# Performance work log

Measured on AMD Instinct MI355X. Metric: run time of the kernel, lower is better.

The kernel has to match this reference:

```python
import jax, jax.numpy as jnp
import numpy as np

N, D_IN = 16384, 1024
E, K = 16, 2
D_EMB, H_UNITS, D_HID = 128, 1024, 512


def setup_inputs() -> dict:
    key = jax.random.key(0)
    ks = jax.random.split(key, 10)
    s = lambda fan_in: 1.0 / np.sqrt(fan_in)
    return {
        "x": jax.random.normal(ks[0], (N, D_IN), jnp.float32),
        "Wr": jax.random.normal(ks[1], (D_IN, D_EMB), jnp.float32) * s(D_IN),
        "br": jnp.zeros((D_EMB,), jnp.float32),
        "expert_embeddings": jax.random.normal(ks[2], (E, D_EMB), jnp.float32) * s(D_EMB),
        "W1": jax.random.normal(ks[3], (E, D_IN, H_UNITS), jnp.float32) * s(D_IN),
        "b1": jnp.zeros((E, H_UNITS), jnp.float32),
        "W2": jax.random.normal(ks[4], (E, H_UNITS, H_UNITS // 2), jnp.float32) * s(H_UNITS),
        "b2": jnp.zeros((E, H_UNITS // 2), jnp.float32),
        "W3": jax.random.normal(ks[5], (E, H_UNITS // 2, D_HID), jnp.float32) * s(H_UNITS // 2),
        "b3": jnp.zeros((E, D_HID), jnp.float32),
    }


def reference(x, Wr, br, expert_embeddings, W1, b1, W2, b2, W3, b3):
    # Router: query per token [N, D_EMB]
    q = x @ Wr + br
    # Negative squared L2 distance to each expert embedding -> scores [N, E]
    d2 = jnp.sum(jnp.square(q[:, None, :] - expert_embeddings[None, :, :]), axis=-1)
    scores = -d2
    # Top-k gating (softmax over the k selected scores only)
    top_k_scores, top_k_idx = jax.lax.top_k(scores, K)        # [N, K]
    gates = jax.nn.softmax(top_k_scores, axis=-1)             # [N, K]
    # Dense all-expert MLP (as the original: every expert on every token)
    h1 = jax.nn.relu(jnp.einsum('nd,edh->enh', x, W1) + b1[:, None, :])   # [E,N,1024]
    h2 = jax.nn.relu(jnp.einsum('enh,ehm->enm', h1, W2) + b2[:, None, :]) # [E,N,512]
    eo = jnp.einsum('enm,emo->eno', h2, W3) + b3[:, None, :]              # [E,N,D_HID]
    eo_t = jnp.transpose(eo, (1, 0, 2))                                   # [N,E,D_HID]
    # Gather top-k expert outputs per token and combine with gates
    sel = jnp.take_along_axis(eo_t, top_k_idx[:, :, None], axis=1)        # [N,K,D_HID]
    combined = jnp.sum(sel * gates[:, :, None], axis=1)                   # [N,D_HID]
    return combined
```

## Files before the change

### kernel.cpp

```cpp
#include <hip/hip_runtime.h>

typedef unsigned short u16;
typedef __attribute__((ext_vector_type(8))) short short8;
typedef __attribute__((ext_vector_type(4))) float f32x4;

#define N_TOK 16384
#define DIN   1024
#define NE    16
#define DEMB  128
#define H1N   1024
#define H2N   512
#define DOUT  512
#define CAP   34816
#define MT    (CAP/128)
#define RBLK  1024

#define OFF_P      0ul
#define OFF_C      65536ul
#define OFF_CTRL   65792ul
#define OFF_E01    66048ul
#define OFF_G01    197120ul
#define OFF_GTOK   328192ul
#define OFF_GGATE  467456ul
#define OFF_TSLOT  606720ul
#define OFF_BH     737792ul
#define OFF_BB     803328ul
#define OFF_W1T    868864ul
#define OFF_W2T    34423296ul
#define OFF_W3T    51200512ul
#define OFF_XBF    59589120ul
#define OFF_H1     93143552ul
#define OFF_H2     164446720ul
#define OFF_EO     OFF_H1

__device__ __forceinline__ u16 f2bf(float f) {
  union { float f; unsigned u; } v; v.f = f;
  unsigned r = v.u + 0x7fff + ((v.u >> 16) & 1);
  return (u16)(r >> 16);
}

__device__ __forceinline__ void async_copy16(const u16* g, u16* l) {
  __builtin_amdgcn_global_load_lds((const __attribute__((address_space(1))) unsigned*)g,
                                   (__attribute__((address_space(3))) unsigned*)l,
                                   16, 0, 0);
}

__global__ void router_prep(const float* __restrict__ Wr, const float* __restrict__ br,
                            const float* __restrict__ emb, float* __restrict__ P,
                            float* __restrict__ c) {
  int idx = blockIdx.x * 256 + threadIdx.x;
  int row = idx >> 4, e = idx & 15;
  float s = 0.f;
  for (int j = 0; j < DEMB; ++j) s += Wr[row * DEMB + j] * emb[e * DEMB + j];
  P[row * NE + e] = 2.f * s;
  if (idx < NE) {
    float cc = 0.f, n2 = 0.f;
    for (int j = 0; j < DEMB; ++j) {
      float ev = emb[idx * DEMB + j];
      cc += br[j] * ev;
      n2 += ev * ev;
    }
    c[idx] = 2.f * cc - n2;
  }
}

__global__ void __launch_bounds__(256) router_score(
    const float* __restrict__ x, const float* __restrict__ P,
    const float* __restrict__ c, int* __restrict__ e01,
    float* __restrict__ g01, int* __restrict__ bhist,
    u16* __restrict__ xbf) {
  __shared__ float xs[16384];
  __shared__ int lh[16];
  int wave = threadIdx.x >> 6, lane = threadIdx.x & 63;
  int e2 = lane & 7, kgl = lane >> 3;
  int tbase = blockIdx.x * 16 + wave * 4;
  float* xw = xs + wave * 4096;

  if (threadIdx.x < 16) lh[threadIdx.x] = 0;

  u16* xbrow = xbf + (size_t)tbase * DIN;
  #pragma unroll
  for (int t = 0; t < 4; ++t) {
    const float* src = x + (size_t)(tbase + t) * DIN;
    #pragma unroll
    for (int q = 0; q < 4; ++q) {
      int g = q * 256 + lane * 4;
      float4 v = *(const float4*)(src + g);
      *(float4*)(xw + t * 1024 + g) = v;
      ushort4 o;
      o.x = f2bf(v.x); o.y = f2bf(v.y); o.z = f2bf(v.z); o.w = f2bf(v.w);
      *(ushort4*)(xbrow + t * DIN + g) = o;
    }
  }
  __syncthreads();

  int te0 = 2 * e2, te1 = te0 + 1;
  float ce0 = c[te0], ce1 = c[te1];
  const float* Pb = P + te0;

  float acc0[4] = {0.f, 0.f, 0.f, 0.f};
  float acc1[4] = {0.f, 0.f, 0.f, 0.f};
  int cbase = kgl * 128;
  #pragma unroll 4
  for (int i = 0; i < 32; ++i) {
    int w = (kgl * 4 + i * 4) & 127;
    int idx = cbase + w;
    float2 pv0 = *(const float2*)(Pb + (size_t)(idx + 0) * NE);
    float2 pv1 = *(const float2*)(Pb + (size_t)(idx + 1) * NE);
    float2 pv2 = *(const float2*)(Pb + (size_t)(idx + 2) * NE);
    float2 pv3 = *(const float2*)(Pb + (size_t)(idx + 3) * NE);
    #pragma unroll
    for (int t = 0; t < 4; ++t) {
      float4 xv = *(const float4*)(xw + t * 1024 + idx);
      acc0[t] = fmaf(xv.x, pv0.x, acc0[t]); acc1[t] = fmaf(xv.x, pv0.y, acc1[t]);
      acc0[t] = fmaf(xv.y, pv1.x, acc0[t]); acc1[t] = fmaf(xv.y, pv1.y, acc1[t]);
      acc0[t] = fmaf(xv.z, pv2.x, acc0[t]); acc1[t] = fmaf(xv.z, pv2.y, acc1[t]);
      acc0[t] = fmaf(xv.w, pv3.x, acc0[t]); acc1[t] = fmaf(xv.w, pv3.y, acc1[t]);
    }
  }

  for (int t = 0; t < 4; ++t) {
    float s0 = acc0[t], s1 = acc1[t];
    #pragma unroll
    for (int off = 8; off <= 32; off <<= 1) {
      s0 += __shfl_xor(s0, off);
      s1 += __shfl_xor(s1, off);
    }
    s0 += ce0; s1 += ce1;
    float hi; int hidx;
    if (s0 >= s1) { hi = s0; hidx = te0; } else { hi = s1; hidx = te1; }
    float m1 = hi; int i1 = hidx;
    #pragma unroll
    for (int off = 1; off < 8; off <<= 1) {
      float so = __shfl_xor(m1, off); int io = __shfl_xor(i1, off);
      if (so > m1 || (so == m1 && io < i1)) { m1 = so; i1 = io; }
    }
    float c2; int c2i;
    if (i1 == te0)      { c2 = s1; c2i = te1; }
    else if (i1 == te1) { c2 = s0; c2i = te0; }
    else                { c2 = hi; c2i = hidx; }
    float m2 = c2; int i2 = c2i;
    #pragma unroll
    for (int off = 1; off < 8; off <<= 1) {
      float so = __shfl_xor(m2, off); int io = __shfl_xor(i2, off);
      if (so > m2 || (so == m2 && io < i2)) { m2 = so; i2 = io; }
    }
    if (lane == 0) {
      int tok = tbase + t;
      float ev = expf(m2 - m1);
      float inv = 1.f / (1.f + ev);
      e01[tok * 2 + 0] = i1; e01[tok * 2 + 1] = i2;
      g01[tok * 2 + 0] = inv; g01[tok * 2 + 1] = ev * inv;
      atomicAdd(&lh[i1], 1);
      atomicAdd(&lh[i2], 1);
    }
  }
  __syncthreads();
  if (threadIdx.x < 16) bhist[blockIdx.x * 16 + threadIdx.x] = lh[threadIdx.x];
}

__global__ void __launch_bounds__(1024) scan_offsets(
    const int* __restrict__ bhist, int* __restrict__ counts,
    int* __restrict__ poff, int* __restrict__ bbase, int* __restrict__ gtok) {
  int t = threadIdx.x;
  int e = t & 15, ch = t >> 4;
  int b0 = ch * 16;
  int s = 0;
  #pragma unroll
  for (int i = 0; i < 16; ++i) s += bhist[(b0 + i) * 16 + e];
  __shared__ int part[64][16];
  __shared__ int chbase[64][16];
  __shared__ int cnt[16];
  __shared__ int pof[16];
  part[ch][e] = s;
  __syncthreads();
  if (t < 16) {
    int run = 0;
    for (int c2 = 0; c2 < 64; ++c2) { chbase[c2][t] = run; run += part[c2][t]; }
    cnt[t] = run;
  }
  __syncthreads();
  if (t == 0) {
    int off = 0;
    for (int e2 = 0; e2 < NE; ++e2) {
      pof[e2] = off;
      poff[e2] = off;
      counts[e2] = cnt[e2];
      off += (cnt[e2] + 127) & ~127;
    }
    poff[NE] = off;
  }
  __syncthreads();
  int padc = ((cnt[e] + 127) & ~127) - cnt[e];
  int pbase = pof[e] + cnt[e];
  if (ch < padc) gtok[pbase + ch] = 0;
  if (ch + 64 < padc) gtok[pbase + ch + 64] = 0;

  int run = pof[e] + chbase[ch][e];
  #pragma unroll
  for (int i = 0; i < 16; ++i) {
    bbase[(b0 + i) * 16 + e] = run;
    run += bhist[(b0 + i) * 16 + e];
  }
}

__global__ void build_lists(const int* __restrict__ e01, const float* __restrict__ g01,
                            const int* __restrict__ bbase, int* __restrict__ gtok,
                            float* __restrict__ ggate, int* __restrict__ tslot) {
  __shared__ int pos[16];
  int tid = threadIdx.x;
  if (tid < 16) pos[tid] = bbase[blockIdx.x * 16 + tid];
  __syncthreads();
  if (tid < 16) {
    int t = blockIdx.x * 16 + tid;
    #pragma unroll
    for (int k = 0; k < 2; ++k) {
      int e = e01[t * 2 + k];
      int p = atomicAdd(&pos[e], 1);
      gtok[p] = t;
      ggate[p] = g01[t * 2 + k];
      tslot[t * 2 + k] = p;
    }
  }
}

template<int K, int N>
__global__ void conv_w(const float* __restrict__ W, u16* __restrict__ WT) {
  __shared__ float tile[64][65];
  int e = blockIdx.z;
  int n0 = blockIdx.x * 64, k0 = blockIdx.y * 64;
  int tx = threadIdx.x & 63, ty = threadIdx.x >> 6;
  const float* Wb = W + (size_t)e * K * N;
  #pragma unroll
  for (int p = 0; p < 16; ++p) {
    int k = p * 4 + ty;
    tile[k][tx] = Wb[(size_t)(k0 + k) * N + n0 + tx];
  }
  __syncthreads();
  u16* WTb = WT + (size_t)e * N * K;
  #pragma unroll
  for (int p = 0; p < 16; ++p) {
    int n = p * 4 + ty;
    WTb[(size_t)(n0 + n) * K + k0 + tx] = f2bf(tile[tx][n]);
  }
}

template<int MODE, bool INDIR>
__global__ void __launch_bounds__(256)
gemm_moe(const u16* __restrict__ A, const u16* __restrict__ Ball,
         const float* __restrict__ bias, u16* __restrict__ Cb, float* __restrict__ outF,
         const int* __restrict__ poff, const int* __restrict__ counts,
         const int* __restrict__ gtok, const float* __restrict__ ggate,
         int K, int N, int nblk) {
  __shared__ u16 Asm[3][4096];
  __shared__ u16 Bsm[3][4096];

  int bid = blockIdx.x;
  int q = nblk >> 3, r = nblk & 7;
  int xcd = bid & 7, sidx = bid >> 3;
  int wg = (xcd < r ? xcd * (q + 1) : r * (q + 1) + (xcd - r) * q) + sidx;
  int NB = N >> 7;
  int rb = wg / NB, nb = wg - rb * NB;

  int row_base = rb * 128;
  if (row_base >= poff[NE]) return;
  int e = 0;
  while (row_base >= poff[e + 1]) ++e;

  int tid = threadIdx.x;
  int wave = tid >> 6, lane = tid & 63;
  int wm = wave >> 1, wn = wave & 1;
  int fr = lane & 15, kq = lane >> 4;
  int n_base = nb * 128;

  const u16* Brow = Ball + (size_t)e * N * K + (size_t)n_base * K;

  int rr0 = tid >> 2, rr1 = rr0 + 64;
  int ch8 = ((tid & 3) ^ ((rr0 >> 1) & 3)) * 8;
  const u16 *a0, *a1;
  if constexpr (INDIR) {
    a0 = A + (size_t)gtok[row_base + rr0] * K;
    a1 = A + (size_t)gtok[row_base + rr1] * K;
  } else {
    a0 = A + (size_t)(row_base + rr0) * K;
    a1 = A + (size_t)(row_base + rr1) * K;
  }
  const u16* b0 = Brow + (size_t)rr0 * K;
  const u16* b1 = Brow + (size_t)rr1 * K;

  f32x4 acc[4][4];
  #pragma unroll
  for (int m = 0; m < 4; ++m)
    #pragma unroll
    for (int n = 0; n < 4; ++n)
      acc[m][n] = (f32x4){0.f, 0.f, 0.f, 0.f};

  int swz = (fr >> 1) & 3;

  auto stage_tile = [&](int buf, int kt) {
    async_copy16(a0 + kt + ch8, &Asm[buf][tid * 8]);
    async_copy16(a1 + kt + ch8, &Asm[buf][(256 + tid) * 8]);
    async_copy16(b0 + kt + ch8, &Bsm[buf][tid * 8]);
    async_copy16(b1 + kt + ch8, &Bsm[buf][(256 + tid) * 8]);
  };

  stage_tile(0, 0);
  stage_tile(1, 32);

  int nstep = K >> 5;
  int rd = 0, st = 2;
  for (int s = 0; s < nstep; ++s) {
    if (s == nstep - 1)
      asm volatile("s_waitcnt vmcnt(0)\n\ts_barrier" ::: "memory");
    else
      asm volatile("s_waitcnt vmcnt(4)\n\ts_barrier" ::: "memory");
    if (s + 2 < nstep) stage_tile(st, (s + 2) << 5);
    short8 av[4], bv[4];
    #pragma unroll
    for (int m = 0; m < 4; ++m)
      av[m] = *(const short8*)(&Asm[rd][((wm * 64 + m * 16 + fr) * 4 + (kq ^ swz)) * 8]);
    #pragma unroll
    for (int n = 0; n < 4; ++n)
      bv[n] = *(const short8*)(&Bsm[rd][((wn * 64 + n * 16 + fr) * 4 + (kq ^ swz)) * 8]);
    #pragma unroll
    for (int m = 0; m < 4; ++m)
      #pragma unroll
      for (int n = 0; n < 4; ++n)
        acc[m][n] = __builtin_amdgcn_mfma_f32_16x16x32_bf16(av[m], bv[n], acc[m][n], 0, 0, 0);
    rd = rd == 2 ? 0 : rd + 1;
    st = st == 2 ? 0 : st + 1;
  }

  int crow = (lane >> 4) * 4;
  int ccol = lane & 15;
  const float* be = bias + (size_t)e * N;
  if constexpr (MODE == 0) {
    #pragma unroll
    for (int m = 0; m < 4; ++m) {
      int gr0 = row_base + wm * 64 + m * 16 + crow;
      #pragma unroll
      for (int n = 0; n < 4; ++n) {
        int gc = n_base + wn * 64 + n * 16 + ccol;
        float bvs = be[gc];
        #pragma unroll
        for (int r2 = 0; r2 < 4; ++r2) {
          float v = acc[m][n][r2] + bvs;
          v = v > 0.f ? v : 0.f;
          Cb[(size_t)(gr0 + r2) * N + gc] = f2bf(v);
        }
      }
    }
  } else {
    #pragma unroll
    for (int m = 0; m < 4; ++m) {
      int gr0 = row_base + wm * 64 + m * 16 + crow;
      #pragma unroll
      for (int n = 0; n < 4; ++n) {
        int gc = n_base + wn * 64 + n * 16 + ccol;
        float bvs = be[gc];
        #pragma unroll
        for (int r2 = 0; r2 < 4; ++r2)
          outF[(size_t)(gr0 + r2) * N + gc] = acc[m][n][r2] + bvs;
      }
    }
  }
}

__global__ void __launch_bounds__(256) combine_out(
    const float* __restrict__ eo, const int* __restrict__ tslot,
    const float* __restrict__ g01, float* __restrict__ out) {
  int wave = threadIdx.x >> 6, lane = threadIdx.x & 63;
  int tok = blockIdx.x * 4 + wave;
  int s0 = tslot[tok * 2 + 0], s1 = tslot[tok * 2 + 1];
  float g0 = g01[tok * 2 + 0], g1 = g01[tok * 2 + 1];
  const float* r0 = eo + (size_t)s0 * DOUT + lane * 8;
  const float* r1 = eo + (size_t)s1 * DOUT + lane * 8;
  float* o = out + (size_t)tok * DOUT + lane * 8;
  #pragma unroll
  for (int j = 0; j < 2; ++j) {
    float4 v0 = ((const float4*)r0)[j];
    float4 v1 = ((const float4*)r1)[j];
    float4 ov;
    ov.x = g0 * v0.x + g1 * v1.x;
    ov.y = g0 * v0.y + g1 * v1.y;
    ov.z = g0 * v0.z + g1 * v1.z;
    ov.w = g0 * v0.w + g1 * v1.w;
    ((float4*)o)[j] = ov;
  }
}

extern "C" void kernel_launch(void* const* d_in, const int* in_sizes, int n_in,
                              void* d_out, int out_size, void* d_ws, size_t ws_size,
                              hipStream_t stream) {
  const float* x   = (const float*)d_in[0];
  const float* Wr  = (const float*)d_in[1];
  const float* br  = (const float*)d_in[2];
  const float* emb = (const float*)d_in[3];
  const float* W1  = (const float*)d_in[4];
  const float* b1  = (const float*)d_in[5];
  const float* W2  = (const float*)d_in[6];
  const float* b2  = (const float*)d_in[7];
  const float* W3  = (const float*)d_in[8];
  const float* b3  = (const float*)d_in[9];
  float* out = (float*)d_out;
  char* ws = (char*)d_ws;

  float* P      = (float*)(ws + OFF_P);
  float* c      = (float*)(ws + OFF_C);
  int*   counts = (int*)(ws + OFF_CTRL);
  int*   poff   = (int*)(ws + OFF_CTRL + 128);
  int*   e01    = (int*)(ws + OFF_E01);
  float* g01    = (float*)(ws + OFF_G01);
  int*   gtok   = (int*)(ws + OFF_GTOK);
  float* ggate  = (float*)(ws + OFF_GGATE);
  int*   tslot  = (int*)(ws + OFF_TSLOT);
  int*   bhist  = (int*)(ws + OFF_BH);
  int*   bbase  = (int*)(ws + OFF_BB);
  u16*   W1T    = (u16*)(ws + OFF_W1T);
  u16*   W2T    = (u16*)(ws + OFF_W2T);
  u16*   W3T    = (u16*)(ws + OFF_W3T);
  u16*   xbf    = (u16*)(ws + OFF_XBF);
  u16*   h1     = (u16*)(ws + OFF_H1);
  u16*   h2     = (u16*)(ws + OFF_H2);
  float* eo     = (float*)(ws + OFF_EO);

  conv_w<DIN, H1N><<<dim3(H1N / 64, DIN / 64, NE), 256, 0, stream>>>(W1, W1T);
  conv_w<H1N, H2N><<<dim3(H2N / 64, H1N / 64, NE), 256, 0, stream>>>(W2, W2T);
  conv_w<H2N, DOUT><<<dim3(DOUT / 64, H2N / 64, NE), 256, 0, stream>>>(W3, W3T);

  router_prep<<<64, 256, 0, stream>>>(Wr, br, emb, P, c);
  router_score<<<RBLK, 256, 0, stream>>>(x, P, c, e01, g01, bhist, xbf);
  scan_offsets<<<1, 1024, 0, stream>>>(bhist, counts, poff, bbase, gtok);
  build_lists<<<RBLK, 64, 0, stream>>>(e01, g01, bbase, gtok, ggate, tslot);

  int nb1 = (H1N / 128) * MT;
  int nb2 = (H2N / 128) * MT;
  int nb3 = (DOUT / 128) * MT;
  gemm_moe<0, true><<<nb1, 256, 0, stream>>>(xbf, W1T, b1, h1, nullptr,
                                             poff, counts, gtok, nullptr, DIN, H1N, nb1);
  gemm_moe<0, false><<<nb2, 256, 0, stream>>>(h1, W2T, b2, h2, nullptr,
                                              poff, counts, nullptr, nullptr, H1N, H2N, nb2);
  gemm_moe<2, false><<<nb3, 256, 0, stream>>>(h2, W3T, b3, nullptr, eo,
                                              poff, counts, nullptr, nullptr, H2N, DOUT, nb3);
  combine_out<<<N_TOK / 4, 256, 0, stream>>>(eo, tslot, g01, out);
}
```

Baseline: 286.5 us.

## Enlarge MoE GEMM tile to 256x128 using 32x32x16 MFMA

Grouped MoE GEMMs now use 256-row M tiles, with each wave computing 128x64 through 32x32x16 bf16 MFMA instead of 16x16x32. The change is meant to raise arithmetic intensity and cut LDS reads per MFMA. Expert segments are padded to 256 rows, which adds padding compute, and the workspace layout is reshuffled so h2 reuses the W1T region. LDS per block grows and the kernel requests two blocks per CU, with fewer blocks in flight for tail balancing.

```diff
diff --git a/kernel.cpp b/kernel.cpp
--- a/kernel.cpp
+++ b/kernel.cpp
@@ -2,7 +2,7 @@
 
 typedef unsigned short u16;
 typedef __attribute__((ext_vector_type(8))) short short8;
-typedef __attribute__((ext_vector_type(4))) float f32x4;
+typedef __attribute__((ext_vector_type(16))) float f32x16;
 
 #define N_TOK 16384
 #define DIN   1024
@@ -11,8 +11,7 @@
 #define H1N   1024
 #define H2N   512
 #define DOUT  512
-#define CAP   34816
-#define MT    (CAP/128)
+#define CAP   36864
 #define RBLK  1024
 
 #define OFF_P      0ul
@@ -21,17 +20,17 @@
 #define OFF_E01    66048ul
 #define OFF_G01    197120ul
 #define OFF_GTOK   328192ul
-#define OFF_GGATE  467456ul
-#define OFF_TSLOT  606720ul
-#define OFF_BH     737792ul
-#define OFF_BB     803328ul
-#define OFF_W1T    868864ul
-#define OFF_W2T    34423296ul
-#define OFF_W3T    51200512ul
-#define OFF_XBF    59589120ul
-#define OFF_H1     93143552ul
-#define OFF_H2     164446720ul
+#define OFF_GGATE  475648ul
+#define OFF_TSLOT  623104ul
+#define OFF_BH     754176ul
+#define OFF_BB     819712ul
+#define OFF_W2T    885248ul
+#define OFF_W3T    17662464ul
+#define OFF_W1T    26051072ul
+#define OFF_XBF    59605504ul
+#define OFF_H1     93159936ul
 #define OFF_EO     OFF_H1
+#define OFF_H2     OFF_W1T
 
 __device__ __forceinline__ u16 f2bf(float f) {
   union { float f; unsigned u; } v; v.f = f;
@@ -186,15 +185,14 @@
       pof[e2] = off;
       poff[e2] = off;
       counts[e2] = cnt[e2];
-      off += (cnt[e2] + 127) & ~127;
+      off += (cnt[e2] + 255) & ~255;
     }
     poff[NE] = off;
   }
   __syncthreads();
-  int padc = ((cnt[e] + 127) & ~127) - cnt[e];
+  int padc = ((cnt[e] + 255) & ~255) - cnt[e];
   int pbase = pof[e] + cnt[e];
-  if (ch < padc) gtok[pbase + ch] = 0;
-  if (ch + 64 < padc) gtok[pbase + ch + 64] = 0;
+  for (int i = ch; i < padc; i += 64) gtok[pbase + i] = 0;
 
   int run = pof[e] + chbase[ch][e];
   #pragma unroll
@@ -246,13 +244,13 @@
 }
 
 template<int MODE, bool INDIR>
-__global__ void __launch_bounds__(256)
+__global__ void __launch_bounds__(256, 2)
 gemm_moe(const u16* __restrict__ A, const u16* __restrict__ Ball,
          const float* __restrict__ bias, u16* __restrict__ Cb, float* __restrict__ outF,
          const int* __restrict__ poff, const int* __restrict__ counts,
          const int* __restrict__ gtok, const float* __restrict__ ggate,
          int K, int N, int nblk) {
-  __shared__ u16 Asm[3][4096];
+  __shared__ u16 Asm[3][8192];
   __shared__ u16 Bsm[3][4096];
 
   int bid = blockIdx.x;
@@ -262,7 +260,7 @@
   int NB = N >> 7;
   int rb = wg / NB, nb = wg - rb * NB;
 
-  int row_base = rb * 128;
+  int row_base = rb * 256;
   if (row_base >= poff[NE]) return;
   int e = 0;
   while (row_base >= poff[e + 1]) ++e;
@@ -270,42 +268,48 @@
   int tid = threadIdx.x;
   int wave = tid >> 6, lane = tid & 63;
   int wm = wave >> 1, wn = wave & 1;
-  int fr = lane & 15, kq = lane >> 4;
   int n_base = nb * 128;
 
   const u16* Brow = Ball + (size_t)e * N * K + (size_t)n_base * K;
 
-  int rr0 = tid >> 2, rr1 = rr0 + 64;
-  int ch8 = ((tid & 3) ^ ((rr0 >> 1) & 3)) * 8;
-  const u16 *a0, *a1;
+  int r0 = tid >> 2;
+  int ch8 = ((tid & 3) ^ ((r0 >> 1) & 3)) * 8;
+  const u16 *a0, *a1, *a2, *a3;
   if constexpr (INDIR) {
-    a0 = A + (size_t)gtok[row_base + rr0] * K;
-    a1 = A + (size_t)gtok[row_base + rr1] * K;
+    a0 = A + (size_t)gtok[row_base + r0 +   0] * K;
+    a1 = A + (size_t)gtok[row_base + r0 +  64] * K;
+    a2 = A + (size_t)gtok[row_base + r0 + 128] * K;
+    a3 = A + (size_t)gtok[row_base + r0 + 192] * K;
   } else {
-    a0 = A + (size_t)(row_base + rr0) * K;
-    a1 = A + (size_t)(row_base + rr1) * K;
-  }
-  const u16* b0 = Brow + (size_t)rr0 * K;
-  const u16* b1 = Brow + (size_t)rr1 * K;
-
-  f32x4 acc[4][4];
+    a0 = A + (size_t)(row_base + r0 +   0) * K;
+    a1 = A + (size_t)(row_base + r0 +  64) * K;
+    a2 = A + (size_t)(row_base + r0 + 128) * K;
+    a3 = A + (size_t)(row_base + r0 + 192) * K;
+  }
+  const u16* b0 = Brow + (size_t)r0 * K;
+  const u16* b1 = Brow + (size_t)(r0 + 64) * K;
+
+  f32x16 acc[4][2];
   #pragma unroll
   for (int m = 0; m < 4; ++m)
     #pragma unroll
-    for (int n = 0; n < 4; ++n)
-      acc[m][n] = (f32x4){0.f, 0.f, 0.f, 0.f};
-
-  int swz = (fr >> 1) & 3;
+    for (int n = 0; n < 2; ++n)
+      acc[m][n] = (f32x16)(0.f);
 
   auto stage_tile = [&](int buf, int kt) {
     async_copy16(a0 + kt + ch8, &Asm[buf][tid * 8]);
     async_copy16(a1 + kt + ch8, &Asm[buf][(256 + tid) * 8]);
+    async_copy16(a2 + kt + ch8, &Asm[buf][(512 + tid) * 8]);
+    async_copy16(a3 + kt + ch8, &Asm[buf][(768 + tid) * 8]);
     async_copy16(b0 + kt + ch8, &Bsm[buf][tid * 8]);
     async_copy16(b1 + kt + ch8, &Bsm[buf][(256 + tid) * 8]);
   };
 
   stage_tile(0, 0);
   stage_tile(1, 32);
+
+  int rowA = lane & 31, hm = lane >> 5;
+  int swzr = (rowA >> 1) & 3;
 
   int nstep = K >> 5;
   int rd = 0, st = 2;
@@ -313,54 +317,54 @@
     if (s == nstep - 1)
       asm volatile("s_waitcnt vmcnt(0)\n\ts_barrier" ::: "memory");
     else
-      asm volatile("s_waitcnt vmcnt(4)\n\ts_barrier" ::: "memory");
+      asm volatile("s_waitcnt vmcnt(6)\n\ts_barrier" ::: "memory");
     if (s + 2 < nstep) stage_tile(st, (s + 2) << 5);
-    short8 av[4], bv[4];
-    #pragma unroll
-    for (int m = 0; m < 4; ++m)
-      av[m] = *(const short8*)(&Asm[rd][((wm * 64 + m * 16 + fr) * 4 + (kq ^ swz)) * 8]);
-    #pragma unroll
-    for (int n = 0; n < 4; ++n)
-      bv[n] = *(const short8*)(&Bsm[rd][((wn * 64 + n * 16 + fr) * 4 + (kq ^ swz)) * 8]);
+    short8 av[4][2], bv[2][2];
     #pragma unroll
     for (int m = 0; m < 4; ++m)
       #pragma unroll
-      for (int n = 0; n < 4; ++n)
-        acc[m][n] = __builtin_amdgcn_mfma_f32_16x16x32_bf16(av[m], bv[n], acc[m][n], 0, 0, 0);
+      for (int s2 = 0; s2 < 2; ++s2)
+        av[m][s2] = *(const short8*)(&Asm[rd][(wm * 128 + m * 32 + rowA) * 32 +
+                                             (((s2 << 1) + hm) ^ swzr) * 8]);
+    #pragma unroll
+    for (int n = 0; n < 2; ++n)
+      #pragma unroll
+      for (int s2 = 0; s2 < 2; ++s2)
+        bv[n][s2] = *(const short8*)(&Bsm[rd][(wn * 64 + n * 32 + rowA) * 32 +
+                                             (((s2 << 1) + hm) ^ swzr) * 8]);
+    #pragma unroll
+    for (int m = 0; m < 4; ++m)
+      #pragma unroll
+      for (int n = 0; n < 2; ++n)
+        #pragma unroll
+        for (int s2 = 0; s2 < 2; ++s2)
+          acc[m][n] = __builtin_amdgcn_mfma_f32_32x32x16_bf16(av[m][s2], bv[n][s2],
+                                                              acc[m][n], 0, 0, 0);
     rd = rd == 2 ? 0 : rd + 1;
     st = st == 2 ? 0 : st + 1;
   }
 
-  int crow = (lane >> 4) * 4;
-  int ccol = lane & 15;
+  int ccol = lane & 31;
+  int crow4 = 4 * hm;
   const float* be = bias + (size_t)e * N;
-  if constexpr (MODE == 0) {
-    #pragma unroll
-    for (int m = 0; m < 4; ++m) {
-      int gr0 = row_base + wm * 64 + m * 16 + crow;
+  #pragma unroll
+  for (int m = 0; m < 4; ++m) {
+    int gr_base = row_base + wm * 128 + m * 32;
+    #pragma unroll
+    for (int n = 0; n < 2; ++n) {
+      int gc = n_base + wn * 64 + n * 32 + ccol;
+      float bvs = be[gc];
       #pragma unroll
-      for (int n = 0; n < 4; ++n) {
-        int gc = n_base + wn * 64 + n * 16 + ccol;
-        float bvs = be[gc];
-        #pragma unroll
-        for (int r2 = 0; r2 < 4; ++r2) {
-          float v = acc[m][n][r2] + bvs;
+      for (int reg = 0; reg < 16; ++reg) {
+        int rowf = (reg & 3) + 8 * (reg >> 2) + crow4;
+        int gr = gr_base + rowf;
+        if constexpr (MODE == 0) {
+          float v = acc[m][n][reg] + bvs;
           v = v > 0.f ? v : 0.f;
-          Cb[(size_t)(gr0 + r2) * N + gc] = f2bf(v);
+          Cb[(size_t)gr * N + gc] = f2bf(v);
+        } else {
+          outF[(size_t)gr * N + gc] = acc[m][n][reg] + bvs;
         }
-      }
-    }
-  } else {
-    #pragma unroll
-    for (int m = 0; m < 4; ++m) {
-      int gr0 = row_base + wm * 64 + m * 16 + crow;
-      #pragma unroll
-      for (int n = 0; n < 4; ++n) {
-        int gc = n_base + wn * 64 + n * 16 + ccol;
-        float bvs = be[gc];
-        #pragma unroll
-        for (int r2 = 0; r2 < 4; ++r2)
-          outF[(size_t)(gr0 + r2) * N + gc] = acc[m][n][r2] + bvs;
       }
     }
   }
@@ -433,9 +437,9 @@
   scan_offsets<<<1, 1024, 0, stream>>>(bhist, counts, poff, bbase, gtok);
   build_lists<<<RBLK, 64, 0, stream>>>(e01, g01, bbase, gtok, ggate, tslot);
 
-  int nb1 = (H1N / 128) * MT;
-  int nb2 = (H2N / 128) * MT;
-  int nb3 = (DOUT / 128) * MT;
+  int nb1 = (H1N / 128) * (CAP / 256);
+  int nb2 = (H2N / 128) * (CAP / 256);
+  int nb3 = (DOUT / 128) * (CAP / 256);
   gemm_moe<0, true><<<nb1, 256, 0, stream>>>(xbf, W1T, b1, h1, nullptr,
                                              poff, counts, gtok, nullptr, DIN, H1N, nb1);
   gemm_moe<0, false><<<nb2, 256, 0, stream>>>(h1, W2T, b2, h2, nullptr,
```

New measurement: 336.7 us. +17.5%, slower.

## Vectorize weight conversion and store expert outputs in bf16 for combine

Applied to the files above, without the earlier changes.

The weight transpose/convert kernel now reads float4 rows and writes 16-byte packed bf16 vectors, replacing scalar loads and 2-byte stores. The last expert GEMM writes its output as bf16 instead of fp32, and the combine kernel reads the bf16 rows and widens them before the gated sum. This cuts global traffic for the weight conversion and for the expert-output round trip. The cost is extra rounding of the final expert outputs to bf16 before gating, which lowers output precision.

```diff
diff --git a/kernel.cpp b/kernel.cpp
--- a/kernel.cpp
+++ b/kernel.cpp
@@ -2,6 +2,7 @@
 
 typedef unsigned short u16;
 typedef __attribute__((ext_vector_type(8))) short short8;
+typedef __attribute__((ext_vector_type(8))) unsigned short ush8;
 typedef __attribute__((ext_vector_type(4))) float f32x4;
 
 #define N_TOK 16384
@@ -39,6 +40,11 @@
   return (u16)(r >> 16);
 }
 
+__device__ __forceinline__ float bf2f(u16 b) {
+  union { unsigned u; float f; } v; v.u = ((unsigned)b) << 16;
+  return v.f;
+}
+
 __device__ __forceinline__ void async_copy16(const u16* g, u16* l) {
   __builtin_amdgcn_global_load_lds((const __attribute__((address_space(1))) unsigned*)g,
                                    (__attribute__((address_space(3))) unsigned*)l,
@@ -225,33 +231,42 @@
 }
 
 template<int K, int N>
-__global__ void conv_w(const float* __restrict__ W, u16* __restrict__ WT) {
+__global__ void __launch_bounds__(256) conv_w(const float* __restrict__ W,
+                                              u16* __restrict__ WT) {
   __shared__ float tile[64][65];
   int e = blockIdx.z;
   int n0 = blockIdx.x * 64, k0 = blockIdx.y * 64;
-  int tx = threadIdx.x & 63, ty = threadIdx.x >> 6;
+  int tid = threadIdx.x;
   const float* Wb = W + (size_t)e * K * N;
-  #pragma unroll
-  for (int p = 0; p < 16; ++p) {
-    int k = p * 4 + ty;
-    tile[k][tx] = Wb[(size_t)(k0 + k) * N + n0 + tx];
-  }
-  __syncthreads();
-  u16* WTb = WT + (size_t)e * N * K;
-  #pragma unroll
-  for (int p = 0; p < 16; ++p) {
-    int n = p * 4 + ty;
-    WTb[(size_t)(n0 + n) * K + k0 + tx] = f2bf(tile[tx][n]);
-  }
+  int kr = tid >> 4, nc = (tid & 15) * 4;
+  #pragma unroll
+  for (int p = 0; p < 4; ++p) {
+    int k = p * 16 + kr;
+    float4 v = *(const float4*)(Wb + (size_t)(k0 + k) * N + n0 + nc);
+    tile[k][nc + 0] = v.x;
+    tile[k][nc + 1] = v.y;
+    tile[k][nc + 2] = v.z;
+    tile[k][nc + 3] = v.w;
+  }
+  __syncthreads();
+  int n = tid >> 2, kc = (tid & 3) * 16;
+  ush8 o0, o1;
+  #pragma unroll
+  for (int j = 0; j < 8; ++j) {
+    o0[j] = f2bf(tile[kc + j][n]);
+    o1[j] = f2bf(tile[kc + 8 + j][n]);
+  }
+  u16* dst = WT + (size_t)e * N * K + (size_t)(n0 + n) * K + k0 + kc;
+  *(ush8*)dst = o0;
+  *(ush8*)(dst + 8) = o1;
 }
 
 template<int MODE, bool INDIR>
 __global__ void __launch_bounds__(256)
 gemm_moe(const u16* __restrict__ A, const u16* __restrict__ Ball,
-         const float* __restrict__ bias, u16* __restrict__ Cb, float* __restrict__ outF,
+         const float* __restrict__ bias, u16* __restrict__ Cb,
          const int* __restrict__ poff, const int* __restrict__ counts,
-         const int* __restrict__ gtok, const float* __restrict__ ggate,
-         int K, int N, int nblk) {
+         const int* __restrict__ gtok, int K, int N, int nblk) {
   __shared__ u16 Asm[3][4096];
   __shared__ u16 Bsm[3][4096];
 
@@ -334,59 +349,44 @@
   int crow = (lane >> 4) * 4;
   int ccol = lane & 15;
   const float* be = bias + (size_t)e * N;
-  if constexpr (MODE == 0) {
-    #pragma unroll
-    for (int m = 0; m < 4; ++m) {
-      int gr0 = row_base + wm * 64 + m * 16 + crow;
+  #pragma unroll
+  for (int m = 0; m < 4; ++m) {
+    int gr0 = row_base + wm * 64 + m * 16 + crow;
+    #pragma unroll
+    for (int n = 0; n < 4; ++n) {
+      int gc = n_base + wn * 64 + n * 16 + ccol;
+      float bvs = be[gc];
       #pragma unroll
-      for (int n = 0; n < 4; ++n) {
-        int gc = n_base + wn * 64 + n * 16 + ccol;
-        float bvs = be[gc];
-        #pragma unroll
-        for (int r2 = 0; r2 < 4; ++r2) {
-          float v = acc[m][n][r2] + bvs;
-          v = v > 0.f ? v : 0.f;
-          Cb[(size_t)(gr0 + r2) * N + gc] = f2bf(v);
-        }
+      for (int r2 = 0; r2 < 4; ++r2) {
+        float v = acc[m][n][r2] + bvs;
+        if constexpr (MODE == 0) v = v > 0.f ? v : 0.f;
+        Cb[(size_t)(gr0 + r2) * N + gc] = f2bf(v);
       }
     }
-  } else {
-    #pragma unroll
-    for (int m = 0; m < 4; ++m) {
-      int gr0 = row_base + wm * 64 + m * 16 + crow;
-      #pragma unroll
-      for (int n = 0; n < 4; ++n) {
-        int gc = n_base + wn * 64 + n * 16 + ccol;
-        float bvs = be[gc];
-        #pragma unroll
-        for (int r2 = 0; r2 < 4; ++r2)
-          outF[(size_t)(gr0 + r2) * N + gc] = acc[m][n][r2] + bvs;
-      }
-    }
   }
 }
 
 __global__ void __launch_bounds__(256) combine_out(
-    const float* __restrict__ eo, const int* __restrict__ tslot,
+    const u16* __restrict__ eo, const int* __restrict__ tslot,
     const float* __restrict__ g01, float* __restrict__ out) {
   int wave = threadIdx.x >> 6, lane = threadIdx.x & 63;
   int tok = blockIdx.x * 4 + wave;
   int s0 = tslot[tok * 2 + 0], s1 = tslot[tok * 2 + 1];
   float g0 = g01[tok * 2 + 0], g1 = g01[tok * 2 + 1];
-  const float* r0 = eo + (size_t)s0 * DOUT + lane * 8;
-  const float* r1 = eo + (size_t)s1 * DOUT + lane * 8;
+  ush8 v0 = *(const ush8*)(eo + (size_t)s0 * DOUT + lane * 8);
+  ush8 v1 = *(const ush8*)(eo + (size_t)s1 * DOUT + lane * 8);
   float* o = out + (size_t)tok * DOUT + lane * 8;
-  #pragma unroll
-  for (int j = 0; j < 2; ++j) {
-    float4 v0 = ((const float4*)r0)[j];
-    float4 v1 = ((const float4*)r1)[j];
-    float4 ov;
-    ov.x = g0 * v0.x + g1 * v1.x;
-    ov.y = g0 * v0.y + g1 * v1.y;
-    ov.z = g0 * v0.z + g1 * v1.z;
-    ov.w = g0 * v0.w + g1 * v1.w;
-    ((float4*)o)[j] = ov;
-  }
+  float4 ov0, ov1;
+  ov0.x = g0 * bf2f(v0[0]) + g1 * bf2f(v1[0]);
+  ov0.y = g0 * bf2f(v0[1]) + g1 * bf2f(v1[1]);
+  ov0.z = g0 * bf2f(v0[2]) + g1 * bf2f(v1[2]);
+  ov0.w = g0 * bf2f(v0[3]) + g1 * bf2f(v1[3]);
+  ov1.x = g0 * bf2f(v0[4]) + g1 * bf2f(v1[4]);
+  ov1.y = g0 * bf2f(v0[5]) + g1 * bf2f(v1[5]);
+  ov1.z = g0 * bf2f(v0[6]) + g1 * bf2f(v1[6]);
+  ov1.w = g0 * bf2f(v0[7]) + g1 * bf2f(v1[7]);
+  ((float4*)o)[0] = ov0;
+  ((float4*)o)[1] = ov1;
 }
 
 extern "C" void kernel_launch(void* const* d_in, const int* in_sizes, int n_in,
@@ -422,7 +422,7 @@
   u16*   xbf    = (u16*)(ws + OFF_XBF);
   u16*   h1     = (u16*)(ws + OFF_H1);
   u16*   h2     = (u16*)(ws + OFF_H2);
-  float* eo     = (float*)(ws + OFF_EO);
+  u16*   eo16   = (u16*)(ws + OFF_EO);
 
   conv_w<DIN, H1N><<<dim3(H1N / 64, DIN / 64, NE), 256, 0, stream>>>(W1, W1T);
   conv_w<H1N, H2N><<<dim3(H2N / 64, H1N / 64, NE), 256, 0, stream>>>(W2, W2T);
@@ -436,11 +436,11 @@
   int nb1 = (H1N / 128) * MT;
   int nb2 = (H2N / 128) * MT;
   int nb3 = (DOUT / 128) * MT;
-  gemm_moe<0, true><<<nb1, 256, 0, stream>>>(xbf, W1T, b1, h1, nullptr,
-                                             poff, counts, gtok, nullptr, DIN, H1N, nb1);
-  gemm_moe<0, false><<<nb2, 256, 0, stream>>>(h1, W2T, b2, h2, nullptr,
-                                              poff, counts, nullptr, nullptr, H1N, H2N, nb2);
-  gemm_moe<2, false><<<nb3, 256, 0, stream>>>(h2, W3T, b3, nullptr, eo,
-                                              poff, counts, nullptr, nullptr, H2N, DOUT, nb3);
-  combine_out<<<N_TOK / 4, 256, 0, stream>>>(eo, tslot, g01, out);
-}
+  gemm_moe<0, true><<<nb1, 256, 0, stream>>>(xbf, W1T, b1, h1,
+                                             poff, counts, gtok, DIN, H1N, nb1);
+  gemm_moe<0, false><<<nb2, 256, 0, stream>>>(h1, W2T, b2, h2,
+                                              poff, counts, nullptr, H1N, H2N, nb2);
+  gemm_moe<2, false><<<nb3, 256, 0, stream>>>(h2, W3T, b3, eo16,
+                                              poff, counts, nullptr, H2N, DOUT, nb3);
+  combine_out<<<N_TOK / 4, 256, 0, stream>>>(eo16, tslot, g01, out);
+}
```

After: 280.2 us (median of 2 runs). -2.2%, faster.
